# Optimization experiments

Measured on AMD Instinct MI355X. Metric: run time of the kernel, lower is better.

## Reference

```python
import jax, jax.numpy as jnp
import numpy as np

N, D, H = 4096, 256, 8
NEG = -4294967295.0  # -2**32 + 1, as in masked_fill


def _layernorm(x, g, b, eps=1e-5):
    mu = jnp.mean(x, axis=-1, keepdims=True)
    var = jnp.var(x, axis=-1, keepdims=True)
    return (x - mu) * jax.lax.rsqrt(var + eps) * g + b


def setup_inputs() -> dict:
    key = jax.random.key(0)
    ks = jax.random.split(key, 12)
    s = 0.02
    return {
        "x": jax.random.normal(ks[0], (N, D), jnp.float32),
        "mask_idx": jax.random.randint(ks[1], (N,), 0, 2, jnp.int32),
        "spatial": jax.random.normal(ks[2], (N, N), jnp.float32),
        "edge": jax.random.normal(ks[3], (N, N), jnp.float32),
        "ln1_g": jnp.ones((D,), jnp.float32),
        "ln1_b": jnp.zeros((D,), jnp.float32),
        "Wq": jax.random.normal(ks[4], (H, D, D), jnp.float32) * s,
        "bq": jnp.zeros((H, D), jnp.float32),
        "Wk": jax.random.normal(ks[5], (H, D, D), jnp.float32) * s,
        "bk": jnp.zeros((H, D), jnp.float32),
        "Wv": jax.random.normal(ks[6], (H, D, D), jnp.float32) * s,
        "bv": jnp.zeros((H, D), jnp.float32),
        "Wo": jax.random.normal(ks[7], (D, H * D), jnp.float32) * s,
        "bo": jnp.zeros((D,), jnp.float32),
        "ln2_g": jnp.ones((D,), jnp.float32),
        "ln2_b": jnp.zeros((D,), jnp.float32),
        "Wff": jax.random.normal(ks[8], (D, D), jnp.float32) * s,
        "bff": jnp.zeros((D,), jnp.float32),
    }


def reference(x, mask_idx, spatial, edge, ln1_g, ln1_b, Wq, bq, Wk, bk, Wv, bv,
              Wo, bo, ln2_g, ln2_b, Wff, bff):
    x_ln = _layernorm(x, ln1_g, ln1_b)
    # per-head projections, torch Linear: y = x W^T + b ; q,k,v: [H, N, D]
    q = jnp.einsum('nd,hed->hne', x_ln, Wq) + bq[:, None, :]
    k = jnp.einsum('nd,hed->hne', x_ln, Wk) + bk[:, None, :]
    v = jnp.einsum('nd,hed->hne', x_ln, Wv) + bv[:, None, :]
    scale = 1.0 / jnp.sqrt(jnp.float32(D))  # dim_q ** 0.5
    a = jnp.einsum('hne,hme->hnm', q, k) * scale  # [H, N, N]
    a = a + spatial[None] + edge[None]
    mask0 = (mask_idx[:, None] * mask_idx[None, :]) == 0  # [N, N]
    a = jnp.where(mask0[None], jnp.float32(NEG), a)
    p = jax.nn.softmax(a, axis=-1)
    p = jnp.where(mask0[None], 0.0, p)
    heads = jnp.einsum('hnm,hme->hne', p, v)  # [H, N, D]
    cat = jnp.transpose(heads, (1, 0, 2)).reshape(N, H * D)
    x_out = cat @ Wo.T + bo + x
    x_attn = _layernorm(x_out, ln2_g, ln2_b) @ Wff.T + bff + x_out
    return x_attn
```

## Files before the change

kernel.cpp:

```cpp
#include <hip/hip_runtime.h>
#include <hip/hip_bf16.h>
#include <hip/hip_fp16.h>
#include <string.h>

typedef unsigned short u16;
typedef __attribute__((ext_vector_type(4))) short short4v;
typedef __attribute__((ext_vector_type(8))) short short8;
typedef __attribute__((ext_vector_type(4))) float floatx4;
typedef __attribute__((ext_vector_type(16))) float floatx16;

#define N_TOK 4096
#define D_DIM 256
#define H_HEAD 8

__device__ __forceinline__ u16 f2b(float f){
  __hip_bfloat16 h = __float2bfloat16(f);
  return *reinterpret_cast<u16*>(&h);
}
__device__ __forceinline__ float b2f(u16 u){
  union { unsigned u; float f; } c; c.u = ((unsigned)u) << 16; return c.f;
}
__device__ __forceinline__ float h2f(u16 u){
  __half h; *reinterpret_cast<u16*>(&h) = u; return __half2float(h);
}
__device__ __forceinline__ u16 f2h(float f){
  __half h = __float2half(f); return *reinterpret_cast<u16*>(&h);
}
__device__ __forceinline__ unsigned pk2bf(float a, float b){
  __hip_bfloat162 h = __float22bfloat162_rn(make_float2(a, b));
  return *reinterpret_cast<unsigned*>(&h);
}

__device__ __forceinline__ void glds16(const void* g, void* l){
  __builtin_amdgcn_global_load_lds(
      (const __attribute__((address_space(1))) unsigned int*)g,
      (__attribute__((address_space(3))) unsigned int*)l, 16, 0, 0);
}

__global__ void fused_prep(const float* __restrict__ Wq, const float* __restrict__ Wk,
                           const float* __restrict__ Wv, const float* __restrict__ Wo,
                           const float* __restrict__ Wff,
                           const float* __restrict__ bq, const float* __restrict__ bk,
                           const float* __restrict__ bv,
                           u16* __restrict__ wqkv, u16* __restrict__ wo_b,
                           u16* __restrict__ wff_b, float* __restrict__ bqkv){
  int bid = blockIdx.x;
  if (bid == 1056){
    int t = threadIdx.x;
    for (int j = 0; j < 24; ++j){
      int idx = t + j*256;
      float v;
      if (idx < 2048) v = bq[idx];
      else if (idx < 4096) v = bk[idx - 2048];
      else v = bv[idx - 4096];
      bqkv[idx] = v;
    }
    return;
  }
  const float* src; u16* dst; int base;
  if      (bid < 256) { src = Wq;  dst = wqkv;            base = bid; }
  else if (bid < 512) { src = Wk;  dst = wqkv + 524288;   base = bid - 256; }
  else if (bid < 768) { src = Wv;  dst = wqkv + 1048576;  base = bid - 512; }
  else if (bid < 1024){ src = Wo;  dst = wo_b;            base = bid - 768; }
  else                { src = Wff; dst = wff_b;           base = bid - 1024; }
  int i = (base*256 + threadIdx.x)*8;
  float4 a = *(const float4*)(src + i);
  float4 b = *(const float4*)(src + i + 4);
  u16 u[8] = {f2b(a.x),f2b(a.y),f2b(a.z),f2b(a.w),f2b(b.x),f2b(b.y),f2b(b.z),f2b(b.w)};
  *(short8*)(dst + i) = *(short8*)u;
}

__global__ void ln_kernel(const float* __restrict__ x, const float* __restrict__ g,
                          const float* __restrict__ b, u16* __restrict__ out){
  const int row = blockIdx.x;
  const int t = threadIdx.x;
  float v = x[(size_t)row*D_DIM + t];
  float s = v, ss = v*v;
  #pragma unroll
  for (int off = 32; off > 0; off >>= 1){
    s  += __shfl_down(s,  off);
    ss += __shfl_down(ss, off);
  }
  __shared__ float ls[4], lss[4];
  const int w = t >> 6, lane = t & 63;
  if (lane == 0){ ls[w] = s; lss[w] = ss; }
  __syncthreads();
  if (t == 0){
    float S  = ls[0]+ls[1]+ls[2]+ls[3];
    float SS = lss[0]+lss[1]+lss[2]+lss[3];
    float mu = S * (1.0f/D_DIM);
    float var = SS * (1.0f/D_DIM) - mu*mu;
    ls[0] = mu; lss[0] = rsqrtf(var + 1e-5f);
  }
  __syncthreads();
  float mu = ls[0], rs = lss[0];
  out[(size_t)row*D_DIM + t] = f2b((v - mu)*rs*g[t] + b[t]);
}

__global__ void ln_sum(const float* __restrict__ p0, const float* __restrict__ p1,
                       const float* __restrict__ bo, const float* __restrict__ x,
                       const float* __restrict__ g, const float* __restrict__ b,
                       float* __restrict__ xout, u16* __restrict__ xln2){
  const int row = blockIdx.x;
  const int t = threadIdx.x;
  const size_t idx = (size_t)row*D_DIM + t;
  float v = p0[idx] + p1[idx] + bo[t] + x[idx];
  float s = v, ss = v*v;
  #pragma unroll
  for (int off = 32; off > 0; off >>= 1){
    s  += __shfl_down(s,  off);
    ss += __shfl_down(ss, off);
  }
  __shared__ float ls[4], lss[4];
  const int w = t >> 6, lane = t & 63;
  if (lane == 0){ ls[w] = s; lss[w] = ss; }
  __syncthreads();
  if (t == 0){
    float S  = ls[0]+ls[1]+ls[2]+ls[3];
    float SS = lss[0]+lss[1]+lss[2]+lss[3];
    float mu = S * (1.0f/D_DIM);
    float var = SS * (1.0f/D_DIM) - mu*mu;
    ls[0] = mu; lss[0] = rsqrtf(var + 1e-5f);
  }
  __syncthreads();
  float mu = ls[0], rs = lss[0];
  xout[idx] = v;
  xln2[idx] = f2b((v - mu)*rs*g[t] + b[t]);
}

__global__ void make_biasW(const float* __restrict__ sp, const float* __restrict__ ed,
                           const int* __restrict__ mask, u16* __restrict__ out){
  __shared__ u16 bh[32][64];
  const int tg = blockIdx.x, q32 = blockIdx.y;
  const int t = threadIdx.x;
  const float L2E = 1.4426950408889634f;
  const u16 NINF = 0xFC00;
  {
    int ql = t>>3, kc = (t&7)*8;
    size_t off = (size_t)(q32*32 + ql)*N_TOK + tg*64 + kc;
    float4 s0 = *(const float4*)(sp + off);
    float4 s1 = *(const float4*)(sp + off + 4);
    float4 e0 = *(const float4*)(ed + off);
    float4 e1 = *(const float4*)(ed + off + 4);
    int mr = mask[q32*32 + ql];
    int4 m0 = *(const int4*)(mask + tg*64 + kc);
    int4 m1 = *(const int4*)(mask + tg*64 + kc + 4);
    bh[ql][kc+0] = (mr*m0.x)==0 ? NINF : f2h((s0.x+e0.x)*L2E);
    bh[ql][kc+1] = (mr*m0.y)==0 ? NINF : f2h((s0.y+e0.y)*L2E);
    bh[ql][kc+2] = (mr*m0.z)==0 ? NINF : f2h((s0.z+e0.z)*L2E);
    bh[ql][kc+3] = (mr*m0.w)==0 ? NINF : f2h((s0.w+e0.w)*L2E);
    bh[ql][kc+4] = (mr*m1.x)==0 ? NINF : f2h((s1.x+e1.x)*L2E);
    bh[ql][kc+5] = (mr*m1.y)==0 ? NINF : f2h((s1.y+e1.y)*L2E);
    bh[ql][kc+6] = (mr*m1.z)==0 ? NINF : f2h((s1.z+e1.z)*L2E);
    bh[ql][kc+7] = (mr*m1.w)==0 ? NINF : f2h((s1.w+e1.w)*L2E);
  }
  __syncthreads();
  int lane2 = t>>2, j0 = (t&3)*8;
  u16 tmp[8];
  #pragma unroll
  for (int jj = 0; jj < 8; ++jj){
    int j = j0 + jj;
    int nb = j>>4, reg = j&15;
    int kvl = nb*32 + (reg&3) + 8*(reg>>2) + 4*(lane2>>5);
    tmp[jj] = bh[lane2&31][kvl];
  }
  u16* dst = out + (((size_t)q32*64 + tg)*64 + lane2)*32 + j0;
  *(short8*)dst = *(short8*)tmp;
}

template<int BM, int BN, int MODE>
__launch_bounds__(256, 2)
__global__ void gemm_bt(const u16* __restrict__ A, const u16* __restrict__ B, int K,
                        int lda, int ldb,
                        const float* __restrict__ bias, const float* __restrict__ resid,
                        void* __restrict__ Cout){
  constexpr int BK = 32;
  constexpr int WM = BM/2, WN = BN/2, FM = WM/16, FN = WN/16;
  constexpr int CApW = BM/64;
  constexpr int CBpW = BN/64;
  __shared__ u16 As[BM*BK];
  __shared__ u16 Bs[BN*BK];
  const int tid = threadIdx.x, w = tid>>6, lane = tid&63;
  const int quad = lane>>4, c16 = lane&15;
  const int wr = w>>1, wc = w&1;
  const int rowT = blockIdx.y*BM, colT = blockIdx.x*BN;
  const int lr = lane>>2;
  const int spos = lane&3;
  const int koff = (MODE == 3) ? (int)blockIdx.z*K : 0;

  floatx4 acc[FM][FN] = {};

  for (int k0 = 0; k0 < K; k0 += BK){
    #pragma unroll
    for (int i = 0; i < CApW; ++i){
      int ch = w*CApW + i;
      int row = ch*16 + lr;
      int gch = spos ^ ((row>>1)&3);
      const u16* g = A + (size_t)(rowT + row)*lda + koff + k0 + gch*8;
      glds16(g, As + ch*512);
    }
    #pragma unroll
    for (int i = 0; i < CBpW; ++i){
      int ch = w*CBpW + i;
      int row = ch*16 + lr;
      int gch = spos ^ ((row>>1)&3);
      const u16* g = B + (size_t)(colT + row)*ldb + koff + k0 + gch*8;
      glds16(g, Bs + ch*512);
    }
    __syncthreads();
    short8 af[FM], bf[FN];
    #pragma unroll
    for (int i = 0; i < FM; ++i){
      int row = wr*WM + i*16 + c16;
      int slot = quad ^ ((row>>1)&3);
      af[i] = *(const short8*)&As[row*BK + slot*8];
    }
    #pragma unroll
    for (int j = 0; j < FN; ++j){
      int row = wc*WN + j*16 + c16;
      int slot = quad ^ ((row>>1)&3);
      bf[j] = *(const short8*)&Bs[row*BK + slot*8];
    }
    #pragma unroll
    for (int i = 0; i < FM; ++i)
      #pragma unroll
      for (int j = 0; j < FN; ++j)
        acc[i][j] = __builtin_amdgcn_mfma_f32_16x16x32_bf16(af[i], bf[j], acc[i][j], 0, 0, 0);
    __syncthreads();
  }

  if (MODE == 0){
    u16* o = (u16*)Cout;
    u16* vtp = (u16*)(size_t)resid;
    #pragma unroll
    for (int i = 0; i < FM; ++i)
      #pragma unroll
      for (int j = 0; j < FN; ++j){
        int col = colT + wc*WN + j*16 + c16;
        float bv = bias[col];
        if (col < 4096){
          float sc = (col < 2048) ? 0.09016994374947424f : 1.0f;
          size_t obase = (size_t)(col>>8)*((size_t)N_TOK*D_DIM) + (col & 255);
          #pragma unroll
          for (int r = 0; r < 4; ++r){
            int row = rowT + wr*WM + i*16 + quad*4 + r;
            o[obase + (size_t)row*D_DIM] = f2b((acc[i][j][r] + bv)*sc);
          }
        } else {
          int row0 = rowT + wr*WM + i*16 + quad*4;
          u16 o4[4];
          #pragma unroll
          for (int r = 0; r < 4; ++r) o4[r] = f2b(acc[i][j][r] + bv);
          *(short4v*)(vtp + (size_t)(col - 4096)*N_TOK + row0) = *(short4v*)o4;
        }
      }
  } else if (MODE == 2){
    float* o = (float*)Cout;
    #pragma unroll
    for (int i = 0; i < FM; ++i)
      #pragma unroll
      for (int j = 0; j < FN; ++j){
        int col = colT + wc*WN + j*16 + c16;
        float bv = bias[col];
        #pragma unroll
        for (int r = 0; r < 4; ++r){
          int row = rowT + wr*WM + i*16 + quad*4 + r;
          size_t idx = (size_t)row*D_DIM + col;
          o[idx] = acc[i][j][r] + bv + resid[idx];
        }
      }
  } else {
    float* o = (float*)Cout + (size_t)blockIdx.z*((size_t)N_TOK*D_DIM);
    #pragma unroll
    for (int i = 0; i < FM; ++i)
      #pragma unroll
      for (int j = 0; j < FN; ++j){
        int col = colT + wc*WN + j*16 + c16;
        #pragma unroll
        for (int r = 0; r < 4; ++r){
          int row = rowT + wr*WM + i*16 + quad*4 + r;
          o[(size_t)row*D_DIM + col] = acc[i][j][r];
        }
      }
  }
}

__launch_bounds__(512, 2)
__global__ void attn_kernel(const u16* __restrict__ Q, const u16* __restrict__ Kg,
                            const u16* __restrict__ Vt, const u16* __restrict__ biasW,
                            u16* __restrict__ cat0, u16* __restrict__ cat1,
                            float* __restrict__ lsum4){
  extern __shared__ __align__(16) u16 lds[];
  u16* Ks = lds;
  u16* Vs = lds + 16384;
  u16* Ps = lds + 32768;
  const int bx = blockIdx.x, h = blockIdx.y, spl = blockIdx.z;
  const int tid = threadIdx.x, w = tid>>6, lane = tid&63;
  const int hi = lane>>5, l31 = lane&31;
  const int qg = w>>1, kvh = w&1;
  const int qh = w&1, ev = w>>1;
  const int qbase = bx*128;
  const size_t hoff = (size_t)h*N_TOK*D_DIM;
  u16* cs = spl ? cat1 : cat0;

  short8 qf[16];
  {
    const u16* qp = Q + hoff + (size_t)(qbase + qg*32 + l31)*D_DIM + hi*8;
    #pragma unroll
    for (int ks = 0; ks < 16; ++ks) qf[ks] = *(const short8*)(qp + ks*16);
  }

  floatx16 o00 = {}, o01 = {}, o10 = {}, o11 = {};
  float l_lane = 0.f;

  const u16* Kb0 = Kg + hoff + (size_t)spl*2048*D_DIM;
  const u16* Vb0 = Vt + hoff + spl*2048;
  const u16* bWb = biasW + ((((size_t)(bx*4 + qg))*64 + spl*32)*64 + lane)*32 + kvh*16;

  short8 bv0 = *(const short8*)(bWb);
  short8 bv1 = *(const short8*)(bWb + 8);
  {
    #pragma unroll
    for (int i = 0; i < 4; ++i){
      int ch = w*4 + i;
      int row = ch*2 + hi;
      int gch = l31 ^ (row&7);
      glds16(Kb0 + (size_t)row*D_DIM + gch*8, Ks + ch*512);
      int vrow = ch*8 + (lane>>3);
      int vgch = (lane&7) ^ (vrow&7);
      glds16(Vb0 + (size_t)vrow*N_TOK + vgch*8, Vs + ch*512);
    }
  }
  __syncthreads();

  for (int t = 0; t < 32; ++t){
    const int tn = (t + 1) & 31;

    floatx16 sa = {}, sb = {};
    const int krow = kvh*32 + l31;
    #pragma unroll
    for (int ks = 0; ks < 16; ++ks){
      int slot = (2*ks + hi) ^ (l31&7);
      short8 ka = *(const short8*)&Ks[krow*256 + slot*8];
      if (ks & 1) sb = __builtin_amdgcn_mfma_f32_32x32x16_bf16(ka, qf[ks], sb, 0, 0, 0);
      else        sa = __builtin_amdgcn_mfma_f32_32x32x16_bf16(ka, qf[ks], sa, 0, 0, 0);
    }

    {
      const int q = qg*32 + l31;
      #pragma unroll
      for (int g = 0; g < 4; ++g){
        u16 b0 = (g < 2) ? ((u16*)&bv0)[4*g+0] : ((u16*)&bv1)[4*(g-2)+0];
        u16 b1 = (g < 2) ? ((u16*)&bv0)[4*g+1] : ((u16*)&bv1)[4*(g-2)+1];
        u16 b2 = (g < 2) ? ((u16*)&bv0)[4*g+2] : ((u16*)&bv1)[4*(g-2)+2];
        u16 b3 = (g < 2) ? ((u16*)&bv0)[4*g+3] : ((u16*)&bv1)[4*(g-2)+3];
        float p0 = exp2f(sa[4*g+0] + sb[4*g+0] + h2f(b0));
        float p1 = exp2f(sa[4*g+1] + sb[4*g+1] + h2f(b1));
        float p2 = exp2f(sa[4*g+2] + sb[4*g+2] + h2f(b2));
        float p3 = exp2f(sa[4*g+3] + sb[4*g+3] + h2f(b3));
        l_lane += (p0 + p1) + (p2 + p3);
        uint2 pw;
        pw.x = pk2bf(p0, p1);
        pw.y = pk2bf(p2, p3);
        int slot = (kvh*4 + g) ^ (l31&7);
        *(uint2*)&Ps[q*64 + slot*8 + hi*4] = pw;
      }
    }
    __syncthreads();

    {
      const u16* Kb = Kb0 + (size_t)tn*64*D_DIM;
      #pragma unroll
      for (int i = 0; i < 4; ++i){
        int ch = w*4 + i;
        int row = ch*2 + hi;
        int gch = l31 ^ (row&7);
        glds16(Kb + (size_t)row*D_DIM + gch*8, Ks + ch*512);
      }
      const u16* bW = bWb + (size_t)tn*64*32;
      bv0 = *(const short8*)(bW);
      bv1 = *(const short8*)(bW + 8);
    }

    #pragma unroll
    for (int ks2 = 0; ks2 < 4; ++ks2){
      int cA = ks2*2 + hi;
      int sl = cA ^ (l31&7);
      short8 pf0 = *(const short8*)&Ps[(qh*64 +      l31)*64 + sl*8];
      short8 pf1 = *(const short8*)&Ps[(qh*64 + 32 + l31)*64 + sl*8];
      short8 vf0 = *(const short8*)&Vs[(ev*64 +      l31)*64 + sl*8];
      short8 vf1 = *(const short8*)&Vs[(ev*64 + 32 + l31)*64 + sl*8];
      o00 = __builtin_amdgcn_mfma_f32_32x32x16_bf16(pf0, vf0, o00, 0, 0, 0);
      o01 = __builtin_amdgcn_mfma_f32_32x32x16_bf16(pf0, vf1, o01, 0, 0, 0);
      o10 = __builtin_amdgcn_mfma_f32_32x32x16_bf16(pf1, vf0, o10, 0, 0, 0);
      o11 = __builtin_amdgcn_mfma_f32_32x32x16_bf16(pf1, vf1, o11, 0, 0, 0);
    }
    __syncthreads();

    {
      const u16* Vb = Vb0 + tn*64;
      #pragma unroll
      for (int i = 0; i < 4; ++i){
        int ch = w*4 + i;
        int vrow = ch*8 + (lane>>3);
        int vgch = (lane&7) ^ (vrow&7);
        glds16(Vb + (size_t)vrow*N_TOK + vgch*8, Vs + ch*512);
      }
    }
  }

  l_lane += __shfl_xor(l_lane, 32, 64);
  if (hi == 0)
    lsum4[(((size_t)spl*2 + kvh)*H_HEAD + h)*N_TOK + qbase + qg*32 + l31] = l_lane;

  #pragma unroll
  for (int reg = 0; reg < 16; ++reg){
    int qr = (reg&3) + 8*(reg>>2) + 4*hi;
    int q0 = qbase + qh*64 + qr;
    size_t c0 = (size_t)q0*(H_HEAD*D_DIM) + h*D_DIM + ev*64 + l31;
    size_t c1 = (size_t)(q0+32)*(H_HEAD*D_DIM) + h*D_DIM + ev*64 + l31;
    cs[c0]      = f2b(o00[reg]);
    cs[c0 + 32] = f2b(o01[reg]);
    cs[c1]      = f2b(o10[reg]);
    cs[c1 + 32] = f2b(o11[reg]);
  }
}

__global__ void combine2(const u16* __restrict__ c0, const u16* __restrict__ c1,
                         const float* __restrict__ lsum4, u16* __restrict__ cat){
  const int q = blockIdx.x;
  const int t = threadIdx.x;
  const int col = t*8;
  const int h = t >> 5;
  float l = 0.f;
  #pragma unroll
  for (int s = 0; s < 4; ++s)
    l += lsum4[((size_t)s*H_HEAD + h)*N_TOK + q];
  float inv = (l > 0.f) ? 1.0f/l : 0.f;
  size_t base = (size_t)q*(H_HEAD*D_DIM) + col;
  short8 a = *(const short8*)(c0 + base);
  short8 b = *(const short8*)(c1 + base);
  u16 o[8];
  #pragma unroll
  for (int i = 0; i < 8; ++i)
    o[i] = f2b((b2f(((u16*)&a)[i]) + b2f(((u16*)&b)[i]))*inv);
  *(short8*)(cat + base) = *(short8*)o;
}

extern "C" void kernel_launch(void* const* d_in, const int* in_sizes, int n_in,
                              void* d_out, int out_size, void* d_ws, size_t ws_size,
                              hipStream_t stream){
  const float* x    = (const float*)d_in[0];
  const int*   mask = (const int*)  d_in[1];
  const float* sp   = (const float*)d_in[2];
  const float* ed   = (const float*)d_in[3];
  const float* g1   = (const float*)d_in[4];
  const float* b1   = (const float*)d_in[5];
  const float* Wq   = (const float*)d_in[6];
  const float* bq   = (const float*)d_in[7];
  const float* Wk   = (const float*)d_in[8];
  const float* bk   = (const float*)d_in[9];
  const float* Wv   = (const float*)d_in[10];
  const float* bv   = (const float*)d_in[11];
  const float* Wo   = (const float*)d_in[12];
  const float* bo   = (const float*)d_in[13];
  const float* g2   = (const float*)d_in[14];
  const float* b2   = (const float*)d_in[15];
  const float* Wff  = (const float*)d_in[16];
  const float* bff  = (const float*)d_in[17];
  float* out = (float*)d_out;
  char* ws = (char*)d_ws;

  constexpr size_t MB = 1ull<<20;
  u16*   wqkv   = (u16*)  (ws + 0);
  u16*   wo_b   = (u16*)  (ws + 3*MB);
  u16*   wff_b  = (u16*)  (ws + 4*MB);
  float* bqkv   = (float*)(ws + 4*MB + 256*1024);
  u16*   xln    = (u16*)  (ws + 4*MB + 512*1024);
  float* lsum4  = (float*)(ws + 6*MB + 512*1024);
  u16*   qkv    = (u16*)  (ws + 7*MB);
  u16*   vt     = (u16*)  (ws + 55*MB);
  u16*   biasW  = (u16*)  (ws + 71*MB);
  u16*   cat0   = (u16*)  (ws + 39*MB);
  u16*   cat1   = (u16*)  (ws + 103*MB);
  u16*   cat    = (u16*)  (ws + 7*MB);
  float* pK     = (float*)(ws + 23*MB);
  float* xout   = (float*)(ws + 31*MB);
  u16*   xln2   = (u16*)  (ws + 35*MB);
  const size_t TS = (size_t)H_HEAD*N_TOK*D_DIM;

  fused_prep<<<1057, 256, 0, stream>>>(Wq, Wk, Wv, Wo, Wff, bq, bk, bv,
                                       wqkv, wo_b, wff_b, bqkv);
  ln_kernel<<<N_TOK, 256, 0, stream>>>(x, g1, b1, xln);

  gemm_bt<128,128,0><<<dim3(48, 32), 256, 0, stream>>>(xln, wqkv, 256, 256, 256,
                                                       bqkv, (const float*)vt, qkv);

  make_biasW<<<dim3(64, 128), 256, 0, stream>>>(sp, ed, mask, biasW);

  hipFuncSetAttribute((const void*)attn_kernel,
                      hipFuncAttributeMaxDynamicSharedMemorySize, 81920);
  attn_kernel<<<dim3(32, 8, 2), 512, 81920, stream>>>(qkv, qkv + TS, vt, biasW,
                                                      cat0, cat1, lsum4);

  combine2<<<N_TOK, 256, 0, stream>>>(cat0, cat1, lsum4, cat);

  gemm_bt<64,64,3><<<dim3(4, 64, 2), 256, 0, stream>>>(cat, wo_b, 1024, 2048, 2048,
                                                       nullptr, nullptr, pK);

  ln_sum<<<N_TOK, 256, 0, stream>>>(pK, pK + (size_t)N_TOK*D_DIM, bo, x, g2, b2,
                                    xout, xln2);

  gemm_bt<64,64,2><<<dim3(4, 64), 256, 0, stream>>>(xln2, wff_b, 256, 256, 256,
                                                    bff, xout, out);
}
```

Before: 419.7 us.

## Drop KV split in attention and normalize output in-kernel, removing combine pass

The attention kernel no longer splits the key range across two blocks. Each block now loops over all 64 key tiles and reduces the row sums through LDS. It normalizes its output directly into the concatenated buffer, which removes the separate combine kernel and its partial buffers. The trade is half as many blocks with twice as long a serial loop, which can leave CUs underused.

After: 403.7 us. 3.8% less time.

```diff
diff --git a/kernel.cpp b/kernel.cpp
--- a/kernel.cpp
+++ b/kernel.cpp
@@ -288,20 +288,18 @@
 __launch_bounds__(512, 2)
 __global__ void attn_kernel(const u16* __restrict__ Q, const u16* __restrict__ Kg,
                             const u16* __restrict__ Vt, const u16* __restrict__ biasW,
-                            u16* __restrict__ cat0, u16* __restrict__ cat1,
-                            float* __restrict__ lsum4){
+                            u16* __restrict__ cat){
   extern __shared__ __align__(16) u16 lds[];
   u16* Ks = lds;
   u16* Vs = lds + 16384;
   u16* Ps = lds + 32768;
-  const int bx = blockIdx.x, h = blockIdx.y, spl = blockIdx.z;
+  const int bx = blockIdx.x, h = blockIdx.y;
   const int tid = threadIdx.x, w = tid>>6, lane = tid&63;
   const int hi = lane>>5, l31 = lane&31;
   const int qg = w>>1, kvh = w&1;
   const int qh = w&1, ev = w>>1;
   const int qbase = bx*128;
   const size_t hoff = (size_t)h*N_TOK*D_DIM;
-  u16* cs = spl ? cat1 : cat0;
 
   short8 qf[16];
   {
@@ -313,9 +311,9 @@
   floatx16 o00 = {}, o01 = {}, o10 = {}, o11 = {};
   float l_lane = 0.f;
 
-  const u16* Kb0 = Kg + hoff + (size_t)spl*2048*D_DIM;
-  const u16* Vb0 = Vt + hoff + spl*2048;
-  const u16* bWb = biasW + ((((size_t)(bx*4 + qg))*64 + spl*32)*64 + lane)*32 + kvh*16;
+  const u16* Kb0 = Kg + hoff;
+  const u16* Vb0 = Vt + hoff;
+  const u16* bWb = biasW + ((((size_t)(bx*4 + qg))*64)*64 + lane)*32 + kvh*16;
 
   short8 bv0 = *(const short8*)(bWb);
   short8 bv1 = *(const short8*)(bWb + 8);
@@ -333,8 +331,8 @@
   }
   __syncthreads();
 
-  for (int t = 0; t < 32; ++t){
-    const int tn = (t + 1) & 31;
+  for (int t = 0; t < 64; ++t){
+    const int tn = t + 1;
 
     floatx16 sa = {}, sb = {};
     const int krow = kvh*32 + l31;
@@ -368,7 +366,7 @@
     }
     __syncthreads();
 
-    {
+    if (t < 63){
       const u16* Kb = Kb0 + (size_t)tn*64*D_DIM;
       #pragma unroll
       for (int i = 0; i < 4; ++i){
@@ -397,7 +395,7 @@
     }
     __syncthreads();
 
-    {
+    if (t < 63){
       const u16* Vb = Vb0 + tn*64;
       #pragma unroll
       for (int i = 0; i < 4; ++i){
@@ -410,41 +408,27 @@
   }
 
   l_lane += __shfl_xor(l_lane, 32, 64);
+  float* lred = (float*)Ps;
   if (hi == 0)
-    lsum4[(((size_t)spl*2 + kvh)*H_HEAD + h)*N_TOK + qbase + qg*32 + l31] = l_lane;
+    lred[kvh*128 + qg*32 + l31] = l_lane;
+  __syncthreads();
 
   #pragma unroll
   for (int reg = 0; reg < 16; ++reg){
     int qr = (reg&3) + 8*(reg>>2) + 4*hi;
-    int q0 = qbase + qh*64 + qr;
+    int q0l = qh*64 + qr;
+    float la = lred[q0l]      + lred[128 + q0l];
+    float lb = lred[q0l + 32] + lred[128 + q0l + 32];
+    float ia = (la > 0.f) ? 1.0f/la : 0.f;
+    float ib = (lb > 0.f) ? 1.0f/lb : 0.f;
+    int q0 = qbase + q0l;
     size_t c0 = (size_t)q0*(H_HEAD*D_DIM) + h*D_DIM + ev*64 + l31;
     size_t c1 = (size_t)(q0+32)*(H_HEAD*D_DIM) + h*D_DIM + ev*64 + l31;
-    cs[c0]      = f2b(o00[reg]);
-    cs[c0 + 32] = f2b(o01[reg]);
-    cs[c1]      = f2b(o10[reg]);
-    cs[c1 + 32] = f2b(o11[reg]);
-  }
-}
-
-__global__ void combine2(const u16* __restrict__ c0, const u16* __restrict__ c1,
-                         const float* __restrict__ lsum4, u16* __restrict__ cat){
-  const int q = blockIdx.x;
-  const int t = threadIdx.x;
-  const int col = t*8;
-  const int h = t >> 5;
-  float l = 0.f;
-  #pragma unroll
-  for (int s = 0; s < 4; ++s)
-    l += lsum4[((size_t)s*H_HEAD + h)*N_TOK + q];
-  float inv = (l > 0.f) ? 1.0f/l : 0.f;
-  size_t base = (size_t)q*(H_HEAD*D_DIM) + col;
-  short8 a = *(const short8*)(c0 + base);
-  short8 b = *(const short8*)(c1 + base);
-  u16 o[8];
-  #pragma unroll
-  for (int i = 0; i < 8; ++i)
-    o[i] = f2b((b2f(((u16*)&a)[i]) + b2f(((u16*)&b)[i]))*inv);
-  *(short8*)(cat + base) = *(short8*)o;
+    cat[c0]      = f2b(o00[reg]*ia);
+    cat[c0 + 32] = f2b(o01[reg]*ia);
+    cat[c1]      = f2b(o10[reg]*ib);
+    cat[c1 + 32] = f2b(o11[reg]*ib);
+  }
 }
 
 extern "C" void kernel_launch(void* const* d_in, const int* in_sizes, int n_in,
@@ -477,13 +461,10 @@
   u16*   wff_b  = (u16*)  (ws + 4*MB);
   float* bqkv   = (float*)(ws + 4*MB + 256*1024);
   u16*   xln    = (u16*)  (ws + 4*MB + 512*1024);
-  float* lsum4  = (float*)(ws + 6*MB + 512*1024);
   u16*   qkv    = (u16*)  (ws + 7*MB);
   u16*   vt     = (u16*)  (ws + 55*MB);
   u16*   biasW  = (u16*)  (ws + 71*MB);
-  u16*   cat0   = (u16*)  (ws + 39*MB);
-  u16*   cat1   = (u16*)  (ws + 103*MB);
-  u16*   cat    = (u16*)  (ws + 7*MB);
+  u16*   cat    = (u16*)  (ws + 103*MB);
   float* pK     = (float*)(ws + 23*MB);
   float* xout   = (float*)(ws + 31*MB);
   u16*   xln2   = (u16*)  (ws + 35*MB);
@@ -500,10 +481,7 @@
 
   hipFuncSetAttribute((const void*)attn_kernel,
                       hipFuncAttributeMaxDynamicSharedMemorySize, 81920);
-  attn_kernel<<<dim3(32, 8, 2), 512, 81920, stream>>>(qkv, qkv + TS, vt, biasW,
-                                                      cat0, cat1, lsum4);
-
-  combine2<<<N_TOK, 256, 0, stream>>>(cat0, cat1, lsum4, cat);
+  attn_kernel<<<dim3(32, 8), 512, 81920, stream>>>(qkv, qkv + TS, vt, biasW, cat);
 
   gemm_bt<64,64,3><<<dim3(4, 64, 2), 256, 0, stream>>>(cat, wo_b, 1024, 2048, 2048,
                                                        nullptr, nullptr, pK);
```
